# Kernel tuning notes

Hardware: AMD Instinct MI355X
Metric: run time of the kernel (lower is better)

## Reference

```python
import jax, jax.numpy as jnp
import numpy as np

NUM_USER = 30000
NUM_ITEM = 30000
N = NUM_USER + NUM_ITEM
DIM = 64          # dim_latent
HID = 4 * DIM     # MLP hidden = 4*dim_latent
E_PAIRS = 500000  # user-item interactions; symmetrized -> 2*E_PAIRS edges
K = 10            # sampling (user-graph neighbors)
B = 2048          # batch_size
DV, DA, DT = 1024, 128, 100


def setup_inputs() -> dict:
    key = jax.random.key(0)
    ks = jax.random.split(key, 24)
    src = jax.random.randint(ks[0], (E_PAIRS,), 0, NUM_USER)
    dst = jax.random.randint(ks[1], (E_PAIRS,), NUM_USER, N)
    # symmetrize like torch.cat((edge, edge[[1,0]]), dim=1)
    edge_index = jnp.stack([jnp.concatenate([src, dst]),
                            jnp.concatenate([dst, src])])  # [2, 2*E_PAIRS]

    def lin_w(k, o, i):
        s = 1.0 / np.sqrt(i)
        return jax.random.uniform(k, (o, i), minval=-s, maxval=s, dtype=jnp.float32)

    return {
        "user_nodes": jax.random.randint(ks[2], (B,), 0, NUM_USER),
        "pos_item_nodes": jax.random.randint(ks[3], (B,), NUM_USER, N),
        "neg_item_nodes": jax.random.randint(ks[4], (B,), NUM_USER, N),
        "user_graph": jax.random.randint(ks[5], (NUM_USER, K), 0, NUM_USER),
        "edge_index": edge_index,
        "user_weight_matrix": jax.nn.softmax(jax.random.normal(ks[6], (NUM_USER, K), dtype=jnp.float32), axis=-1),
        "v_feat": jax.random.normal(ks[7], (NUM_ITEM, DV), dtype=jnp.float32),
        "a_feat": jax.random.normal(ks[8], (NUM_ITEM, DA), dtype=jnp.float32),
        "t_feat": jax.random.normal(ks[9], (NUM_ITEM, DT), dtype=jnp.float32),
        "v_pref": 0.1 * jax.random.normal(ks[10], (NUM_USER, DIM), dtype=jnp.float32),
        "a_pref": 0.1 * jax.random.normal(ks[11], (NUM_USER, DIM), dtype=jnp.float32),
        "t_pref": 0.1 * jax.random.normal(ks[12], (NUM_USER, DIM), dtype=jnp.float32),
        "v_W1": lin_w(ks[13], HID, DV), "v_b1": jnp.zeros((HID,), jnp.float32),
        "v_W2": lin_w(ks[14], DIM, HID), "v_b2": jnp.zeros((DIM,), jnp.float32),
        "a_W1": lin_w(ks[15], HID, DA), "a_b1": jnp.zeros((HID,), jnp.float32),
        "a_W2": lin_w(ks[16], DIM, HID), "a_b2": jnp.zeros((DIM,), jnp.float32),
        "t_W1": lin_w(ks[17], HID, DT), "t_b1": jnp.zeros((HID,), jnp.float32),
        "t_W2": lin_w(ks[18], DIM, HID), "t_b2": jnp.zeros((DIM,), jnp.float32),
        "weight_u": jax.nn.softmax(jax.random.normal(ks[19], (NUM_USER, 3, 1), dtype=jnp.float32), axis=1),
    }


def _l2norm(x):
    # F.normalize(x): rowwise L2 with eps=1e-12
    return x / jnp.maximum(jnp.linalg.norm(x, axis=-1, keepdims=True), 1e-12)


def _gcn_conv(x, src, dst, dinv):
    # Base_gcn(aggr='add'): out[i] = sum_{e: dst_e=i} dinv[src_e]*dinv[dst_e]*x[src_e]
    norm = dinv[src] * dinv[dst]
    return jax.ops.segment_sum(norm[:, None] * x[src], dst, num_segments=N)


def _modality(feat, pref, W1, b1, W2, b2, src, dst, dinv):
    # GCN.forward (Movielens branch, dim_latent=64)
    temp = jax.nn.leaky_relu(feat @ W1.T + b1) @ W2.T + b2  # MLP_1(leaky_relu(MLP(f)))
    x = _l2norm(jnp.concatenate([pref, temp], axis=0))       # [N, DIM]
    h = _gcn_conv(x, src, dst, dinv)
    h1 = _gcn_conv(h, src, dst, dinv)
    return h + x + h1


def reference(user_nodes, pos_item_nodes, neg_item_nodes, user_graph, edge_index,
              user_weight_matrix, v_feat, a_feat, t_feat,
              v_pref, a_pref, t_pref,
              v_W1, v_b1, v_W2, v_b2,
              a_W1, a_b1, a_W2, a_b2,
              t_W1, t_b1, t_W2, t_b2, weight_u):
    src, dst = edge_index[0], edge_index[1]
    deg = jax.ops.segment_sum(jnp.ones_like(src, dtype=jnp.float32), src, num_segments=N)
    dinv = jnp.where(deg > 0, deg ** -0.5, 0.0)

    v_rep = _modality(v_feat, v_pref, v_W1, v_b1, v_W2, v_b2, src, dst, dinv)
    a_rep = _modality(a_feat, a_pref, a_W1, a_b1, a_W2, a_b2, src, dst, dinv)
    t_rep = _modality(t_feat, t_pref, t_W1, t_b1, t_W2, t_b2, src, dst, dinv)

    representation = (v_rep + a_rep + t_rep) / 3.0
    # weighted_sum construction: per-user learned modality weights [U,3,1]
    user_stack = jnp.stack([v_rep[:NUM_USER], a_rep[:NUM_USER], t_rep[:NUM_USER]], axis=2)  # [U, D, 3]
    user_rep = jnp.einsum('udm,umo->ud', user_stack, weight_u)
    item_rep = representation[NUM_USER:]

    # User_Graph_sample: weighted sum over k sampled user neighbors
    h_u1 = jnp.einsum('uk,ukd->ud', user_weight_matrix, user_rep[user_graph])
    user_rep = user_rep + h_u1

    result = jnp.concatenate([user_rep, item_rep], axis=0)  # [N, DIM]
    u = result[user_nodes]
    pos_scores = jnp.sum(u * result[pos_item_nodes], axis=1)
    neg_scores = jnp.sum(u * result[neg_item_nodes], axis=1)
    return pos_scores, neg_scores
```

## Files before the change

### kernel.cpp

```cpp
#include <hip/hip_runtime.h>
#include <hip/hip_bf16.h>
#include <math.h>

#define NUSER 30000
#define NITEM 30000
#define NN    60000
#define NE    1000000
#define DIMV  64
#define XW    192
#define HIDW  256
#define NB    2048
#define KNB   10
#define MPAD  30080
#define NCH   235

typedef __attribute__((ext_vector_type(8))) short bf16x8;
typedef __attribute__((ext_vector_type(4))) float f32x4;

__device__ __forceinline__ short f2bf(float f) {
    union { float f; unsigned u; } v; v.f = f;
    unsigned r = v.u + 0x7fff + ((v.u >> 16) & 1);
    return (short)(r >> 16);
}
__device__ __forceinline__ float bflo(unsigned v) { return __int_as_float(v << 16); }
__device__ __forceinline__ float bfhi(unsigned v) { return __int_as_float(v & 0xffff0000u); }
__device__ __forceinline__ unsigned pack2(float a, float b) {
    return (unsigned)(unsigned short)f2bf(a) | ((unsigned)(unsigned short)f2bf(b) << 16);
}
__device__ __forceinline__ void async16(void* lds, const void* g) {
    __builtin_amdgcn_global_load_lds(
        (const __attribute__((address_space(1))) unsigned*)g,
        (__attribute__((address_space(3))) unsigned*)lds, 16, 0, 0);
}

__global__ void k_deg(const int* __restrict__ src, unsigned* __restrict__ deg) {
    int e = blockIdx.x * blockDim.x + threadIdx.x;
    if (e < NE) atomicAdd(&deg[src[e]], 1u);
}
__global__ void k_dinv(const unsigned* __restrict__ deg, float* __restrict__ dinv) {
    int i = blockIdx.x * blockDim.x + threadIdx.x;
    if (i < NN) { unsigned d = deg[i]; dinv[i] = d ? rsqrtf((float)d) : 0.f; }
}
__global__ __launch_bounds__(256)
void k_bsum(const unsigned* __restrict__ deg, int* __restrict__ bsum) {
    __shared__ int red[4];
    int g = blockIdx.x * 256 + threadIdx.x;
    int v = (g < NN) ? (int)deg[g] : 0;
    for (int o = 32; o > 0; o >>= 1) v += __shfl_down(v, o);
    int lane = threadIdx.x & 63, wave = threadIdx.x >> 6;
    if (lane == 0) red[wave] = v;
    __syncthreads();
    if (threadIdx.x == 0) bsum[blockIdx.x] = red[0] + red[1] + red[2] + red[3];
}
__global__ __launch_bounds__(256)
void k_bscan(const int* __restrict__ bsum, int* __restrict__ bscan) {
    __shared__ int s[256];
    int t = threadIdx.x;
    int v = (t < NCH) ? bsum[t] : 0;
    s[t] = v;
    __syncthreads();
    for (int o = 1; o < 256; o <<= 1) {
        int u = (t >= o) ? s[t - o] : 0;
        __syncthreads();
        s[t] += u;
        __syncthreads();
    }
    if (t < NCH) bscan[t] = s[t] - v;
}
__global__ __launch_bounds__(256)
void k_rowptr(const unsigned* __restrict__ deg, const int* __restrict__ bscan,
              int* __restrict__ rowptr) {
    __shared__ int s[256];
    int g = blockIdx.x * 256 + threadIdx.x, t = threadIdx.x;
    int v = (g < NN) ? (int)deg[g] : 0;
    s[t] = v;
    __syncthreads();
    for (int o = 1; o < 256; o <<= 1) {
        int u = (t >= o) ? s[t - o] : 0;
        __syncthreads();
        s[t] += u;
        __syncthreads();
    }
    int base = bscan[blockIdx.x];
    if (g < NN) rowptr[g] = base + s[t] - v;
    if (g == NN - 1) rowptr[NN] = base + s[t];
}
__global__ void k_fill(const int* __restrict__ src, const int* __restrict__ dst,
                       const float* __restrict__ dinv, const int* __restrict__ rowptr,
                       unsigned* __restrict__ cursor, int2* __restrict__ csr) {
    int e = blockIdx.x * blockDim.x + threadIdx.x;
    if (e >= NE) return;
    int s = src[e], d = dst[e];
    int pos = (int)atomicAdd(&cursor[d], 1u);
    int2 ew;
    ew.x = s;
    ew.y = __float_as_int(dinv[s] * dinv[d]);
    csr[rowptr[d] + pos] = ew;
}

struct CvtArgs { const float* src[6]; short* dst[6]; };
__constant__ __device__ const int C8PRE[7]  = {0,32768,36864,40960,43008,45056,47104};
__constant__ __device__ const int C8SH[6]   = {7,4,4,5,5,5};
__constant__ __device__ const int C8COLS[6] = {1024,128,100,256,256,256};
__constant__ __device__ const int C8ROWS[6] = {256,256,256,64,64,64};
#define CVT8_TOTAL 47104

__global__ __launch_bounds__(256)
void k_convert(CvtArgs a) {
    int cid = blockIdx.x * 256 + threadIdx.x;
    if (cid >= CVT8_TOTAL) return;
    int j = 0;
    while (cid >= C8PRE[j + 1]) ++j;
    int local = cid - C8PRE[j];
    int sh = C8SH[j];
    int r = local >> sh;
    int col = (local & ((1 << sh) - 1)) * 8;
    int cols = C8COLS[j];
    bf16x8 o = (bf16x8)0;
    if (r < C8ROWS[j]) {
        const float* s = a.src[j] + (size_t)r * cols + col;
        if (col + 8 <= cols) {
            float4 f0 = *(const float4*)s;
            float4 f1 = *(const float4*)(s + 4);
            o[0] = f2bf(f0.x); o[1] = f2bf(f0.y); o[2] = f2bf(f0.z); o[3] = f2bf(f0.w);
            o[4] = f2bf(f1.x); o[5] = f2bf(f1.y); o[6] = f2bf(f1.z); o[7] = f2bf(f1.w);
        } else {
            #pragma unroll
            for (int q = 0; q < 8; ++q)
                if (col + q < cols) o[q] = f2bf(s[q]);
        }
    }
    *(bf16x8*)(a.dst[j] + ((size_t)r << (sh + 3)) + col) = o;
}

__device__ __forceinline__ bf16x8 ldfrag(const short* lds, int row, int kbyte) {
    int off = (row * 128 + kbyte) ^ ((row & 7) << 4);
    return *(const bf16x8*)((const char*)lds + off);
}
#define STAGE_TILE(SMEM, BASEPTR, LDK, ROWOFF, K0, NITERS)                          \
    _Pragma("unroll")                                                                \
    for (int i_ = 0; i_ < (NITERS); ++i_) {                                          \
        int c_ = i_ * 256 + wave * 64 + lane;                                        \
        int r_ = c_ >> 3, slot_ = c_ & 7;                                            \
        int ss_ = slot_ ^ (r_ & 7);                                                  \
        const char* gp_ = (const char*)((BASEPTR) + (size_t)((ROWOFF) + r_) * (LDK)  \
                                        + (K0)) + ss_ * 16;                          \
        async16(&(SMEM)[(i_ * 256 + wave * 64) * 8], gp_);                           \
    }

struct G1Args { const float* A[3]; const short* W[3]; const float* bias[3];
                short* C[3]; int K[3]; int Ksrc[3]; };
__global__ __launch_bounds__(256)
void gemm1_mfma(G1Args g) {
    __shared__ __align__(16) short sA[64 * 64];
    __shared__ __align__(16) short sB[128 * 64];
    int m = blockIdx.z;
    int K  = g.K[m];
    int Ks = g.Ksrc[m];
    const float* A = g.A[m];
    const short* W = g.W[m];
    int tid = threadIdx.x;
    int lane = tid & 63, wave = tid >> 6;
    int wr = wave >> 1, wc = wave & 1;
    int lane15 = lane & 15, lhi = lane >> 4;
    int row0 = blockIdx.x * 64, col0 = blockIdx.y * 128;
    int srow = tid >> 2, sc16 = tid & 3;
    int grow = row0 + srow;
    bool rowok = grow < NITEM;
    const float* arow = A + (size_t)grow * Ks + sc16 * 16;
    int nt = K >> 6;
    float4 f[4];
    auto loadA = [&](int t) {
        int k0 = t * 64;
        int gk = k0 + sc16 * 16;
        if (rowok && gk + 16 <= Ks) {
            #pragma unroll
            for (int q = 0; q < 4; ++q) f[q] = *(const float4*)(arow + k0 + q * 4);
        } else {
            #pragma unroll
            for (int q = 0; q < 4; ++q) {
                float4 z = make_float4(0.f, 0.f, 0.f, 0.f);
                if (rowok) {
                    int c = gk + q * 4;
                    if (c + 4 <= Ks) {
                        z = *(const float4*)(arow + k0 + q * 4);
                    } else {
                        if (c + 0 < Ks) z.x = arow[k0 + q * 4 + 0];
                        if (c + 1 < Ks) z.y = arow[k0 + q * 4 + 1];
                        if (c + 2 < Ks) z.z = arow[k0 + q * 4 + 2];
                        if (c + 3 < Ks) z.w = arow[k0 + q * 4 + 3];
                    }
                }
                f[q] = z;
            }
        }
    };
    loadA(0);
    f32x4 acc[2][4] = {};
    for (int t = 0; t < nt; ++t) {
        #pragma unroll
        for (int q = 0; q < 2; ++q) {
            bf16x8 o;
            float4 lo = f[q * 2], hi = f[q * 2 + 1];
            o[0] = f2bf(lo.x); o[1] = f2bf(lo.y); o[2] = f2bf(lo.z); o[3] = f2bf(lo.w);
            o[4] = f2bf(hi.x); o[5] = f2bf(hi.y); o[6] = f2bf(hi.z); o[7] = f2bf(hi.w);
            int c8 = sc16 * 2 + q;
            int off = (srow * 128 + c8 * 16) ^ ((srow & 7) << 4);
            *(bf16x8*)((char*)sA + off) = o;
        }
        int k0 = t * 64;
        STAGE_TILE(sB, W, K, col0, k0, 4)
        __syncthreads();
        if (t + 1 < nt) loadA(t + 1);
        #pragma unroll
        for (int ks = 0; ks < 2; ++ks) {
            int kb = ks * 64 + lhi * 16;
            bf16x8 a[2], b[4];
            #pragma unroll
            for (int mi = 0; mi < 2; ++mi) a[mi] = ldfrag(sA, wr * 32 + mi * 16 + lane15, kb);
            #pragma unroll
            for (int ni = 0; ni < 4; ++ni) b[ni] = ldfrag(sB, wc * 64 + ni * 16 + lane15, kb);
            #pragma unroll
            for (int mi = 0; mi < 2; ++mi)
                #pragma unroll
                for (int ni = 0; ni < 4; ++ni)
                    acc[mi][ni] = __builtin_amdgcn_mfma_f32_16x16x32_bf16(a[mi], b[ni], acc[mi][ni], 0, 0, 0);
        }
        __syncthreads();
    }
    short* C = g.C[m];
    const float* bias = g.bias[m];
    #pragma unroll
    for (int mi = 0; mi < 2; ++mi) {
        int grow0 = row0 + wr * 32 + mi * 16 + lhi * 4;
        #pragma unroll
        for (int ni = 0; ni < 4; ++ni) {
            int gcol = col0 + wc * 64 + ni * 16 + lane15;
            float bv = bias[gcol];
            #pragma unroll
            for (int r = 0; r < 4; ++r) {
                float v = acc[mi][ni][r] + bv;
                v = v > 0.f ? v : 0.01f * v;
                C[(size_t)(grow0 + r) * HIDW + gcol] = f2bf(v);
            }
        }
    }
}

struct G2Args { const short* A[3]; const short* W[3]; const float* bias[3]; };
__global__ __launch_bounds__(256)
void gemm2_mfma(G2Args g, float* __restrict__ X, short* __restrict__ Xb) {
    __shared__ __align__(16) short sA[128 * 64];
    __shared__ __align__(16) short sB[64 * 64];
    int m = blockIdx.z;
    const short* A = g.A[m];
    const short* W = g.W[m];
    int lane = threadIdx.x & 63, wave = threadIdx.x >> 6;
    int lane15 = lane & 15, lhi = lane >> 4;
    int row0 = blockIdx.x * 128;
    const int K = HIDW;
    f32x4 acc[2][4] = {};
    for (int t = 0; t < 4; ++t) {
        int k0 = t * 64;
        STAGE_TILE(sA, A, K, row0, k0, 4)
        STAGE_TILE(sB, W, K, 0, k0, 2)
        __syncthreads();
        #pragma unroll
        for (int ks = 0; ks < 2; ++ks) {
            int kb = ks * 64 + lhi * 16;
            bf16x8 a[2], b[4];
            #pragma unroll
            for (int mi = 0; mi < 2; ++mi) a[mi] = ldfrag(sA, wave * 32 + mi * 16 + lane15, kb);
            #pragma unroll
            for (int ni = 0; ni < 4; ++ni) b[ni] = ldfrag(sB, ni * 16 + lane15, kb);
            #pragma unroll
            for (int mi = 0; mi < 2; ++mi)
                #pragma unroll
                for (int ni = 0; ni < 4; ++ni)
                    acc[mi][ni] = __builtin_amdgcn_mfma_f32_16x16x32_bf16(a[mi], b[ni], acc[mi][ni], 0, 0, 0);
        }
        __syncthreads();
    }
    const float* bias = g.bias[m];
    #pragma unroll
    for (int mi = 0; mi < 2; ++mi) {
        float v[4][4];
        float sumsq[4] = {};
        #pragma unroll
        for (int ni = 0; ni < 4; ++ni) {
            float bv = bias[ni * 16 + lane15];
            #pragma unroll
            for (int r = 0; r < 4; ++r) {
                float x = acc[mi][ni][r] + bv;
                v[ni][r] = x;
                sumsq[r] += x * x;
            }
        }
        #pragma unroll
        for (int r = 0; r < 4; ++r) {
            float s = sumsq[r];
            s += __shfl_xor(s, 1); s += __shfl_xor(s, 2);
            s += __shfl_xor(s, 4); s += __shfl_xor(s, 8);
            sumsq[r] = 1.f / fmaxf(sqrtf(s), 1e-12f);
        }
        int grow0 = row0 + wave * 32 + mi * 16 + lhi * 4;
        #pragma unroll
        for (int r = 0; r < 4; ++r) {
            int grow = grow0 + r;
            if (grow < NITEM) {
                float sc = sumsq[r];
                size_t o = (size_t)(NUSER + grow) * XW + m * DIMV;
                #pragma unroll
                for (int ni = 0; ni < 4; ++ni) {
                    float val = v[ni][r] * sc;
                    X[o + ni * 16 + lane15] = val;
                    Xb[o + ni * 16 + lane15] = f2bf(val);
                }
            }
        }
    }
}

__global__ void k_users_norm(const float* __restrict__ vp, const float* __restrict__ ap,
                             const float* __restrict__ tp, float* __restrict__ X,
                             short* __restrict__ Xb) {
    int gw = (blockIdx.x * blockDim.x + threadIdx.x) >> 6;
    int lane = threadIdx.x & 63;
    if (gw >= NUSER * 3) return;
    int u = gw / 3, m = gw % 3;
    const float* p = (m == 0) ? vp : (m == 1) ? ap : tp;
    float v = p[(size_t)u * DIMV + lane];
    float s = v * v;
    for (int o = 32; o > 0; o >>= 1) s += __shfl_xor(s, o);
    float sc = 1.f / fmaxf(sqrtf(s), 1e-12f);
    size_t o = (size_t)u * XW + m * DIMV + lane;
    float val = v * sc;
    X[o] = val;
    Xb[o] = f2bf(val);
}

template<int MODE>
__global__ __launch_bounds__(256)
void k_spmm(const int* __restrict__ rowptr, const int2* __restrict__ csr,
            const short* __restrict__ INB, const float* __restrict__ Xf,
            float* __restrict__ OUTf, short* __restrict__ OUTB) {
    int n = blockIdx.x * 4 + (threadIdx.x >> 6);
    int l = threadIdx.x & 63;
    if (n >= NN) return;
    int lo = rowptr[n], hi = rowptr[n + 1];
    int lc = l < 48 ? l : 47;
    float f0 = 0.f, f1 = 0.f, f2 = 0.f, f3 = 0.f;
    for (int base = lo; base < hi; base += 64) {
        int idx = base + l;
        int2 e = (idx < hi) ? csr[idx] : make_int2(0, 0);
        int m = hi - base; if (m > 64) m = 64;
        int j = 0;
        for (; j + 4 <= m; j += 4) {
            int s0 = __builtin_amdgcn_readlane(e.x, j + 0);
            int s1 = __builtin_amdgcn_readlane(e.x, j + 1);
            int s2 = __builtin_amdgcn_readlane(e.x, j + 2);
            int s3 = __builtin_amdgcn_readlane(e.x, j + 3);
            float w0 = __int_as_float(__builtin_amdgcn_readlane(e.y, j + 0));
            float w1 = __int_as_float(__builtin_amdgcn_readlane(e.y, j + 1));
            float w2 = __int_as_float(__builtin_amdgcn_readlane(e.y, j + 2));
            float w3 = __int_as_float(__builtin_amdgcn_readlane(e.y, j + 3));
            uint2 v0 = ((const uint2*)(INB + (size_t)s0 * XW))[lc];
            uint2 v1 = ((const uint2*)(INB + (size_t)s1 * XW))[lc];
            uint2 v2 = ((const uint2*)(INB + (size_t)s2 * XW))[lc];
            uint2 v3 = ((const uint2*)(INB + (size_t)s3 * XW))[lc];
            f0 += w0 * bflo(v0.x); f1 += w0 * bfhi(v0.x);
            f2 += w0 * bflo(v0.y); f3 += w0 * bfhi(v0.y);
            f0 += w1 * bflo(v1.x); f1 += w1 * bfhi(v1.x);
            f2 += w1 * bflo(v1.y); f3 += w1 * bfhi(v1.y);
            f0 += w2 * bflo(v2.x); f1 += w2 * bfhi(v2.x);
            f2 += w2 * bflo(v2.y); f3 += w2 * bfhi(v2.y);
            f0 += w3 * bflo(v3.x); f1 += w3 * bfhi(v3.x);
            f2 += w3 * bflo(v3.y); f3 += w3 * bfhi(v3.y);
        }
        for (; j < m; ++j) {
            int s0 = __builtin_amdgcn_readlane(e.x, j);
            float w0 = __int_as_float(__builtin_amdgcn_readlane(e.y, j));
            uint2 v0 = ((const uint2*)(INB + (size_t)s0 * XW))[lc];
            f0 += w0 * bflo(v0.x); f1 += w0 * bfhi(v0.x);
            f2 += w0 * bflo(v0.y); f3 += w0 * bfhi(v0.y);
        }
    }
    if (MODE == 1) {
        float4 xv = ((const float4*)(Xf + (size_t)n * XW))[lc];
        uint2 hb = ((const uint2*)(INB + (size_t)n * XW))[lc];
        f0 += xv.x + bflo(hb.x); f1 += xv.y + bfhi(hb.x);
        f2 += xv.z + bflo(hb.y); f3 += xv.w + bfhi(hb.y);
    }
    if (l < 48) {
        if (MODE == 0) {
            uint2 ob;
            ob.x = pack2(f0, f1);
            ob.y = pack2(f2, f3);
            ((uint2*)(OUTB + (size_t)n * XW))[l] = ob;
        } else {
            ((float4*)(OUTf + (size_t)n * XW))[l] = make_float4(f0, f1, f2, f3);
        }
    }
}

__global__ void k_combine(const float* __restrict__ REP, const float* __restrict__ wu,
                          float* __restrict__ UR, float* __restrict__ RES) {
    int t = blockIdx.x * blockDim.x + threadIdx.x;
    if (t >= NN * DIMV) return;
    int n = t >> 6, d = t & 63;
    const float* r = REP + (size_t)n * XW;
    float r0 = r[d], r1 = r[DIMV + d], r2 = r[2 * DIMV + d];
    if (n < NUSER) {
        float w0 = wu[n * 3 + 0], w1 = wu[n * 3 + 1], w2 = wu[n * 3 + 2];
        UR[(size_t)n * DIMV + d] = r0 * w0 + r1 * w1 + r2 * w2;
    } else {
        RES[(size_t)n * DIMV + d] = (r0 + r1 + r2) * (1.f / 3.f);
    }
}
__global__ void k_usergraph(const float* __restrict__ UR, const int* __restrict__ g,
                            const float* __restrict__ w, float* __restrict__ RES) {
    int t = blockIdx.x * blockDim.x + threadIdx.x;
    if (t >= NUSER * DIMV) return;
    int n = t >> 6, d = t & 63;
    float acc = UR[(size_t)n * DIMV + d];
    for (int k = 0; k < KNB; ++k) {
        int nb = g[n * KNB + k];
        acc += w[n * KNB + k] * UR[(size_t)nb * DIMV + d];
    }
    RES[(size_t)n * DIMV + d] = acc;
}
__global__ void k_scores(const float* __restrict__ RES, const int* __restrict__ un,
                         const int* __restrict__ pn, const int* __restrict__ nn,
                         float* __restrict__ out) {
    int gw = (blockIdx.x * blockDim.x + threadIdx.x) >> 6;
    int lane = threadIdx.x & 63;
    if (gw >= NB) return;
    int u = un[gw], p = pn[gw], ng = nn[gw];
    float uv = RES[(size_t)u * DIMV + lane];
    float ps = uv * RES[(size_t)p * DIMV + lane];
    float ns = uv * RES[(size_t)ng * DIMV + lane];
    for (int o = 32; o > 0; o >>= 1) {
        ps += __shfl_xor(ps, o);
        ns += __shfl_xor(ns, o);
    }
    if (lane == 0) { out[gw] = ps; out[NB + gw] = ns; }
}

extern "C" void kernel_launch(void* const* d_in, const int* in_sizes, int n_in,
                              void* d_out, int out_size, void* d_ws, size_t ws_size,
                              hipStream_t stream) {
    const int*   un    = (const int*)d_in[0];
    const int*   pn    = (const int*)d_in[1];
    const int*   ngn   = (const int*)d_in[2];
    const int*   ug    = (const int*)d_in[3];
    const int*   eidx  = (const int*)d_in[4];
    const float* uwm   = (const float*)d_in[5];
    const float* feats[3] = { (const float*)d_in[6], (const float*)d_in[7], (const float*)d_in[8] };
    const float* prefs[3] = { (const float*)d_in[9], (const float*)d_in[10], (const float*)d_in[11] };
    const float* W1[3] = { (const float*)d_in[12], (const float*)d_in[16], (const float*)d_in[20] };
    const float* b1[3] = { (const float*)d_in[13], (const float*)d_in[17], (const float*)d_in[21] };
    const float* W2[3] = { (const float*)d_in[14], (const float*)d_in[18], (const float*)d_in[22] };
    const float* b2[3] = { (const float*)d_in[15], (const float*)d_in[19], (const float*)d_in[23] };
    const float* wu    = (const float*)d_in[24];
    float* out = (float*)d_out;

    const int* esrc = eidx;
    const int* edst = eidx + NE;

    char* ws = (char*)d_ws;
    size_t off = 0;
    auto alloc = [&](size_t bytes) { void* p = ws + off; off = (off + bytes + 255) & ~(size_t)255; return p; };
    unsigned* deg    = (unsigned*)alloc(NN * 4);
    float*    dinv   = (float*)alloc(NN * 4);
    int*      rowptr = (int*)alloc((NN + 1) * 4);
    int*      bsum   = (int*)alloc(NCH * 4);
    int*      bscan  = (int*)alloc(NCH * 4);
    int2*     csr    = (int2*)alloc((size_t)NE * 8);
    float*    X      = (float*)alloc((size_t)NN * XW * 4);
    short*    Xb     = (short*)alloc((size_t)NN * XW * 2);
    char* region2 = (char*)alloc((size_t)3 * MPAD * HIDW * 2);
    short* hid[3] = { (short*)region2,
                      (short*)(region2 + (size_t)MPAD * HIDW * 2),
                      (short*)(region2 + (size_t)2 * MPAD * HIDW * 2) };
    float* RES = (float*)region2;
    float* UR  = (float*)(region2 + (size_t)NN * DIMV * 4 + 40960);
    short* Hb  = (short*)(region2 + (size_t)NN * DIMV * 4 + 40960 + (size_t)NUSER * DIMV * 4);
    short* w1b = (short*)alloc((size_t)256 * 1280 * 2);
    short* w1s[3] = { w1b, w1b + 256 * 1024, w1b + 256 * (1024 + 128) };
    short* w2b = (short*)alloc((size_t)3 * 64 * HIDW * 2);
    short* w2s[3] = { w2b, w2b + 64 * HIDW, w2b + 2 * 64 * HIDW };

    CvtArgs ca;
    ca.src[0] = W1[0]; ca.src[1] = W1[1]; ca.src[2] = W1[2];
    ca.src[3] = W2[0]; ca.src[4] = W2[1]; ca.src[5] = W2[2];
    ca.dst[0] = w1s[0]; ca.dst[1] = w1s[1]; ca.dst[2] = w1s[2];
    ca.dst[3] = w2s[0]; ca.dst[4] = w2s[1]; ca.dst[5] = w2s[2];
    k_convert<<<(CVT8_TOTAL + 255) / 256, 256, 0, stream>>>(ca);

    hipMemsetAsync(deg, 0, NN * 4, stream);
    k_deg<<<(NE + 255) / 256, 256, 0, stream>>>(esrc, deg);
    k_dinv<<<(NN + 255) / 256, 256, 0, stream>>>(deg, dinv);
    k_bsum<<<NCH, 256, 0, stream>>>(deg, bsum);
    k_bscan<<<1, 256, 0, stream>>>(bsum, bscan);
    k_rowptr<<<NCH, 256, 0, stream>>>(deg, bscan, rowptr);
    hipMemsetAsync(deg, 0, NN * 4, stream);
    k_fill<<<(NE + 255) / 256, 256, 0, stream>>>(esrc, edst, dinv, rowptr, deg, csr);

    G1Args g1;
    for (int m = 0; m < 3; ++m) { g1.bias[m] = b1[m]; g1.C[m] = hid[m]; g1.W[m] = w1s[m]; g1.A[m] = feats[m]; }
    g1.K[0] = 1024; g1.K[1] = 128; g1.K[2] = 128;
    g1.Ksrc[0] = 1024; g1.Ksrc[1] = 128; g1.Ksrc[2] = 100;
    gemm1_mfma<<<dim3(MPAD / 64, 2, 3), 256, 0, stream>>>(g1);

    G2Args g2;
    for (int m = 0; m < 3; ++m) { g2.A[m] = hid[m]; g2.W[m] = w2s[m]; g2.bias[m] = b2[m]; }
    gemm2_mfma<<<dim3(MPAD / 128, 1, 3), 256, 0, stream>>>(g2, X, Xb);
    k_users_norm<<<(NUSER * 3 * 64 + 255) / 256, 256, 0, stream>>>(prefs[0], prefs[1], prefs[2], X, Xb);

    k_spmm<0><<<(NN + 3) / 4, 256, 0, stream>>>(rowptr, csr, Xb, nullptr, nullptr, Hb);

    k_spmm<1><<<(NN + 3) / 4, 256, 0, stream>>>(rowptr, csr, Hb, X, X, nullptr);

    k_combine<<<(NN * DIMV + 255) / 256, 256, 0, stream>>>(X, wu, UR, RES);
    k_usergraph<<<(NUSER * DIMV + 255) / 256, 256, 0, stream>>>(UR, ug, uwm, RES);
    k_scores<<<(NB * 64 + 255) / 256, 256, 0, stream>>>(RES, un, pn, ngn, out);
}
```

Before: 343.7 us.

## Double-buffer LDS tiles in gemm1 to overlap staging with MFMA compute

```diff
diff --git a/kernel.cpp b/kernel.cpp
--- a/kernel.cpp
+++ b/kernel.cpp
@@ -152,8 +152,8 @@
                 short* C[3]; int K[3]; int Ksrc[3]; };
 __global__ __launch_bounds__(256)
 void gemm1_mfma(G1Args g) {
-    __shared__ __align__(16) short sA[64 * 64];
-    __shared__ __align__(16) short sB[128 * 64];
+    __shared__ __align__(16) short sA[2][64 * 64];
+    __shared__ __align__(16) short sB[2][128 * 64];
     int m = blockIdx.z;
     int K  = g.K[m];
     int Ks = g.Ksrc[m];
@@ -195,9 +195,7 @@
             }
         }
     };
-    loadA(0);
-    f32x4 acc[2][4] = {};
-    for (int t = 0; t < nt; ++t) {
+    auto writeA = [&](short* dst) {
         #pragma unroll
         for (int q = 0; q < 2; ++q) {
             bf16x8 o;
@@ -206,27 +204,46 @@
             o[4] = f2bf(hi.x); o[5] = f2bf(hi.y); o[6] = f2bf(hi.z); o[7] = f2bf(hi.w);
             int c8 = sc16 * 2 + q;
             int off = (srow * 128 + c8 * 16) ^ ((srow & 7) << 4);
-            *(bf16x8*)((char*)sA + off) = o;
-        }
-        int k0 = t * 64;
-        STAGE_TILE(sB, W, K, col0, k0, 4)
-        __syncthreads();
-        if (t + 1 < nt) loadA(t + 1);
+            *(bf16x8*)((char*)dst + off) = o;
+        }
+    };
+    f32x4 acc[2][4] = {};
+    auto compute = [&](int buf) {
         #pragma unroll
         for (int ks = 0; ks < 2; ++ks) {
             int kb = ks * 64 + lhi * 16;
             bf16x8 a[2], b[4];
             #pragma unroll
-            for (int mi = 0; mi < 2; ++mi) a[mi] = ldfrag(sA, wr * 32 + mi * 16 + lane15, kb);
-            #pragma unroll
-            for (int ni = 0; ni < 4; ++ni) b[ni] = ldfrag(sB, wc * 64 + ni * 16 + lane15, kb);
+            for (int mi = 0; mi < 2; ++mi) a[mi] = ldfrag(sA[buf], wr * 32 + mi * 16 + lane15, kb);
+            #pragma unroll
+            for (int ni = 0; ni < 4; ++ni) b[ni] = ldfrag(sB[buf], wc * 64 + ni * 16 + lane15, kb);
             #pragma unroll
             for (int mi = 0; mi < 2; ++mi)
                 #pragma unroll
                 for (int ni = 0; ni < 4; ++ni)
                     acc[mi][ni] = __builtin_amdgcn_mfma_f32_16x16x32_bf16(a[mi], b[ni], acc[mi][ni], 0, 0, 0);
         }
-        __syncthreads();
+    };
+    loadA(0);
+    writeA(sA[0]);
+    STAGE_TILE(sB[0], W, K, col0, 0, 4)
+    if (nt > 1) loadA(1);
+    asm volatile("s_waitcnt vmcnt(4) lgkmcnt(0)" ::: "memory");
+    __builtin_amdgcn_s_barrier();
+    for (int t = 0; t < nt; ++t) {
+        int cur = t & 1, nxt = cur ^ 1;
+        bool more = (t + 1 < nt);
+        if (more) {
+            writeA(sA[nxt]);
+            STAGE_TILE(sB[nxt], W, K, col0, (t + 1) * 64, 4)
+            if (t + 2 < nt) loadA(t + 2);
+        }
+        compute(cur);
+        if (more) {
+            if (t + 2 < nt) asm volatile("s_waitcnt vmcnt(4) lgkmcnt(0)" ::: "memory");
+            else            asm volatile("s_waitcnt vmcnt(0) lgkmcnt(0)" ::: "memory");
+            __builtin_amdgcn_s_barrier();
+        }
     }
     short* C = g.C[m];
     const float* bias = g.bias[m];
```

New measurement: 351.8 us. 2.3% more time.

## Fuse MLP layer-1 and layer-2 GEMMs, keeping hidden activations in LDS

Applied to the files above, without the earlier changes.

```diff
diff --git a/kernel.cpp b/kernel.cpp
--- a/kernel.cpp
+++ b/kernel.cpp
@@ -137,6 +137,10 @@
     int off = (row * 128 + kbyte) ^ ((row & 7) << 4);
     return *(const bf16x8*)((const char*)lds + off);
 }
+__device__ __forceinline__ bf16x8 ldfrag512(const short* lds, int row, int kbyte) {
+    int off = (row * 512 + kbyte) ^ ((row & 7) << 4);
+    return *(const bf16x8*)((const char*)lds + off);
+}
 #define STAGE_TILE(SMEM, BASEPTR, LDK, ROWOFF, K0, NITERS)                          \
     _Pragma("unroll")                                                                \
     for (int i_ = 0; i_ < (NITERS); ++i_) {                                          \
@@ -148,26 +152,27 @@
         async16(&(SMEM)[(i_ * 256 + wave * 64) * 8], gp_);                           \
     }
 
-struct G1Args { const float* A[3]; const short* W[3]; const float* bias[3];
-                short* C[3]; int K[3]; int Ksrc[3]; };
+struct G12Args { const float* A[3]; const short* W1[3]; const float* b1[3];
+                 const short* W2[3]; const float* b2[3]; int K[3]; int Ksrc[3]; };
 __global__ __launch_bounds__(256)
-void gemm1_mfma(G1Args g) {
+void gemm12_mfma(G12Args g, float* __restrict__ X, short* __restrict__ Xb) {
     __shared__ __align__(16) short sA[64 * 64];
-    __shared__ __align__(16) short sB[128 * 64];
+    __shared__ __align__(16) short sB[256 * 64];
+    short* sHid = sB;
     int m = blockIdx.z;
     int K  = g.K[m];
     int Ks = g.Ksrc[m];
-    const float* A = g.A[m];
-    const short* W = g.W[m];
+    const float* A  = g.A[m];
+    const short* W1 = g.W1[m];
     int tid = threadIdx.x;
     int lane = tid & 63, wave = tid >> 6;
     int wr = wave >> 1, wc = wave & 1;
     int lane15 = lane & 15, lhi = lane >> 4;
-    int row0 = blockIdx.x * 64, col0 = blockIdx.y * 128;
+    int row0 = blockIdx.x * 64;
     int srow = tid >> 2, sc16 = tid & 3;
-    int grow = row0 + srow;
-    bool rowok = grow < NITEM;
-    const float* arow = A + (size_t)grow * Ks + sc16 * 16;
+    int grow_s = row0 + srow;
+    bool rowok = grow_s < NITEM;
+    const float* arow = A + (size_t)grow_s * Ks + sc16 * 16;
     int nt = K >> 6;
     float4 f[4];
     auto loadA = [&](int t) {
@@ -196,7 +201,7 @@
         }
     };
     loadA(0);
-    f32x4 acc[2][4] = {};
+    f32x4 acc[2][8] = {};
     for (int t = 0; t < nt; ++t) {
         #pragma unroll
         for (int q = 0; q < 2; ++q) {
@@ -208,114 +213,88 @@
             int off = (srow * 128 + c8 * 16) ^ ((srow & 7) << 4);
             *(bf16x8*)((char*)sA + off) = o;
         }
-        int k0 = t * 64;
-        STAGE_TILE(sB, W, K, col0, k0, 4)
+        STAGE_TILE(sB, W1, K, 0, t * 64, 8)
         __syncthreads();
         if (t + 1 < nt) loadA(t + 1);
         #pragma unroll
         for (int ks = 0; ks < 2; ++ks) {
             int kb = ks * 64 + lhi * 16;
-            bf16x8 a[2], b[4];
+            bf16x8 a[2], b[8];
             #pragma unroll
             for (int mi = 0; mi < 2; ++mi) a[mi] = ldfrag(sA, wr * 32 + mi * 16 + lane15, kb);
             #pragma unroll
-            for (int ni = 0; ni < 4; ++ni) b[ni] = ldfrag(sB, wc * 64 + ni * 16 + lane15, kb);
+            for (int ni = 0; ni < 8; ++ni) b[ni] = ldfrag(sB, wc * 128 + ni * 16 + lane15, kb);
             #pragma unroll
             for (int mi = 0; mi < 2; ++mi)
                 #pragma unroll
-                for (int ni = 0; ni < 4; ++ni)
+                for (int ni = 0; ni < 8; ++ni)
                     acc[mi][ni] = __builtin_amdgcn_mfma_f32_16x16x32_bf16(a[mi], b[ni], acc[mi][ni], 0, 0, 0);
         }
         __syncthreads();
     }
-    short* C = g.C[m];
-    const float* bias = g.bias[m];
+    const float* b1 = g.b1[m];
     #pragma unroll
     for (int mi = 0; mi < 2; ++mi) {
-        int grow0 = row0 + wr * 32 + mi * 16 + lhi * 4;
+        int rh0 = wr * 32 + mi * 16 + lhi * 4;
         #pragma unroll
-        for (int ni = 0; ni < 4; ++ni) {
-            int gcol = col0 + wc * 64 + ni * 16 + lane15;
-            float bv = bias[gcol];
+        for (int ni = 0; ni < 8; ++ni) {
+            int ch = wc * 128 + ni * 16 + lane15;
+            float bv = b1[ch];
             #pragma unroll
             for (int r = 0; r < 4; ++r) {
                 float v = acc[mi][ni][r] + bv;
                 v = v > 0.f ? v : 0.01f * v;
-                C[(size_t)(grow0 + r) * HIDW + gcol] = f2bf(v);
+                int rh = rh0 + r;
+                int off = (rh * 512 + ch * 2) ^ ((rh & 7) << 4);
+                *(short*)((char*)sHid + off) = f2bf(v);
             }
         }
     }
-}
-
-struct G2Args { const short* A[3]; const short* W[3]; const float* bias[3]; };
-__global__ __launch_bounds__(256)
-void gemm2_mfma(G2Args g, float* __restrict__ X, short* __restrict__ Xb) {
-    __shared__ __align__(16) short sA[128 * 64];
-    __shared__ __align__(16) short sB[64 * 64];
-    int m = blockIdx.z;
-    const short* A = g.A[m];
-    const short* W = g.W[m];
-    int lane = threadIdx.x & 63, wave = threadIdx.x >> 6;
-    int lane15 = lane & 15, lhi = lane >> 4;
-    int row0 = blockIdx.x * 128;
-    const int K = HIDW;
-    f32x4 acc[2][4] = {};
-    for (int t = 0; t < 4; ++t) {
-        int k0 = t * 64;
-        STAGE_TILE(sA, A, K, row0, k0, 4)
-        STAGE_TILE(sB, W, K, 0, k0, 2)
-        __syncthreads();
-        #pragma unroll
-        for (int ks = 0; ks < 2; ++ks) {
-            int kb = ks * 64 + lhi * 16;
-            bf16x8 a[2], b[4];
-            #pragma unroll
-            for (int mi = 0; mi < 2; ++mi) a[mi] = ldfrag(sA, wave * 32 + mi * 16 + lane15, kb);
-            #pragma unroll
-            for (int ni = 0; ni < 4; ++ni) b[ni] = ldfrag(sB, ni * 16 + lane15, kb);
-            #pragma unroll
-            for (int mi = 0; mi < 2; ++mi)
-                #pragma unroll
-                for (int ni = 0; ni < 4; ++ni)
-                    acc[mi][ni] = __builtin_amdgcn_mfma_f32_16x16x32_bf16(a[mi], b[ni], acc[mi][ni], 0, 0, 0);
-        }
-        __syncthreads();
-    }
-    const float* bias = g.bias[m];
+    __syncthreads();
+    const short* W2 = g.W2[m];
+    const short* bp2 = W2 + (size_t)lane15 * HIDW + lhi * 8;
+    f32x4 acc2[4] = {};
     #pragma unroll
-    for (int mi = 0; mi < 2; ++mi) {
-        float v[4][4];
-        float sumsq[4] = {};
+    for (int k0 = 0; k0 < HIDW; k0 += 32) {
+        bf16x8 a2 = ldfrag512(sHid, wave * 16 + lane15, k0 * 2 + lhi * 16);
         #pragma unroll
         for (int ni = 0; ni < 4; ++ni) {
-            float bv = bias[ni * 16 + lane15];
-            #pragma unroll
-            for (int r = 0; r < 4; ++r) {
-                float x = acc[mi][ni][r] + bv;
-                v[ni][r] = x;
-                sumsq[r] += x * x;
-            }
-        }
+            bf16x8 b2 = *(const bf16x8*)(bp2 + (size_t)ni * 16 * HIDW + k0);
+            acc2[ni] = __builtin_amdgcn_mfma_f32_16x16x32_bf16(a2, b2, acc2[ni], 0, 0, 0);
+        }
+    }
+    const float* b2 = g.b2[m];
+    float v2[4][4];
+    float sumsq[4] = {};
+    #pragma unroll
+    for (int ni = 0; ni < 4; ++ni) {
+        float bv = b2[ni * 16 + lane15];
         #pragma unroll
         for (int r = 0; r < 4; ++r) {
-            float s = sumsq[r];
-            s += __shfl_xor(s, 1); s += __shfl_xor(s, 2);
-            s += __shfl_xor(s, 4); s += __shfl_xor(s, 8);
-            sumsq[r] = 1.f / fmaxf(sqrtf(s), 1e-12f);
-        }
-        int grow0 = row0 + wave * 32 + mi * 16 + lhi * 4;
-        #pragma unroll
-        for (int r = 0; r < 4; ++r) {
-            int grow = grow0 + r;
-            if (grow < NITEM) {
-                float sc = sumsq[r];
-                size_t o = (size_t)(NUSER + grow) * XW + m * DIMV;
-                #pragma unroll
-                for (int ni = 0; ni < 4; ++ni) {
-                    float val = v[ni][r] * sc;
-                    X[o + ni * 16 + lane15] = val;
-                    Xb[o + ni * 16 + lane15] = f2bf(val);
-                }
+            float x = acc2[ni][r] + bv;
+            v2[ni][r] = x;
+            sumsq[r] += x * x;
+        }
+    }
+    #pragma unroll
+    for (int r = 0; r < 4; ++r) {
+        float s = sumsq[r];
+        s += __shfl_xor(s, 1); s += __shfl_xor(s, 2);
+        s += __shfl_xor(s, 4); s += __shfl_xor(s, 8);
+        sumsq[r] = 1.f / fmaxf(sqrtf(s), 1e-12f);
+    }
+    int grow0 = row0 + wave * 16 + lhi * 4;
+    #pragma unroll
+    for (int r = 0; r < 4; ++r) {
+        int grow = grow0 + r;
+        if (grow < NITEM) {
+            float sc = sumsq[r];
+            size_t o = (size_t)(NUSER + grow) * XW + m * DIMV;
+            #pragma unroll
+            for (int ni = 0; ni < 4; ++ni) {
+                float val = v2[ni][r] * sc;
+                X[o + ni * 16 + lane15] = val;
+                Xb[o + ni * 16 + lane15] = f2bf(val);
             }
         }
     }
@@ -479,9 +458,6 @@
     float*    X      = (float*)alloc((size_t)NN * XW * 4);
     short*    Xb     = (short*)alloc((size_t)NN * XW * 2);
     char* region2 = (char*)alloc((size_t)3 * MPAD * HIDW * 2);
-    short* hid[3] = { (short*)region2,
-                      (short*)(region2 + (size_t)MPAD * HIDW * 2),
-                      (short*)(region2 + (size_t)2 * MPAD * HIDW * 2) };
     float* RES = (float*)region2;
     float* UR  = (float*)(region2 + (size_t)NN * DIMV * 4 + 40960);
     short* Hb  = (short*)(region2 + (size_t)NN * DIMV * 4 + 40960 + (size_t)NUSER * DIMV * 4);
@@ -506,15 +482,14 @@
     hipMemsetAsync(deg, 0, NN * 4, stream);
     k_fill<<<(NE + 255) / 256, 256, 0, stream>>>(esrc, edst, dinv, rowptr, deg, csr);
 
-    G1Args g1;
-    for (int m = 0; m < 3; ++m) { g1.bias[m] = b1[m]; g1.C[m] = hid[m]; g1.W[m] = w1s[m]; g1.A[m] = feats[m]; }
-    g1.K[0] = 1024; g1.K[1] = 128; g1.K[2] = 128;
-    g1.Ksrc[0] = 1024; g1.Ksrc[1] = 128; g1.Ksrc[2] = 100;
-    gemm1_mfma<<<dim3(MPAD / 64, 2, 3), 256, 0, stream>>>(g1);
-
-    G2Args g2;
-    for (int m = 0; m < 3; ++m) { g2.A[m] = hid[m]; g2.W[m] = w2s[m]; g2.bias[m] = b2[m]; }
-    gemm2_mfma<<<dim3(MPAD / 128, 1, 3), 256, 0, stream>>>(g2, X, Xb);
+    G12Args g12;
+    for (int m = 0; m < 3; ++m) {
+        g12.A[m] = feats[m]; g12.W1[m] = w1s[m]; g12.b1[m] = b1[m];
+        g12.W2[m] = w2s[m];  g12.b2[m] = b2[m];
+    }
+    g12.K[0] = 1024; g12.K[1] = 128; g12.K[2] = 128;
+    g12.Ksrc[0] = 1024; g12.Ksrc[1] = 128; g12.Ksrc[2] = 100;
+    gemm12_mfma<<<dim3(MPAD / 64, 1, 3), 256, 0, stream>>>(g12, X, Xb);
     k_users_norm<<<(NUSER * 3 * 64 + 255) / 256, 256, 0, stream>>>(prefs[0], prefs[1], prefs[2], X, Xb);
 
     k_spmm<0><<<(NN + 3) / 4, 256, 0, stream>>>(rowptr, csr, Xb, nullptr, nullptr, Hb);
```

Measured after the change: 341.9 us. Within noise of the previous version (-0.5%).
